# Performance work log

Hardware: AMD Instinct MI355X
Metric: run time of the kernel (lower is better)

Reference implementation:

```python
import jax, jax.numpy as jnp
import numpy as np


def setup_inputs() -> dict:
    key = jax.random.key(0)
    ks = jax.random.split(key, 10)
    B, T, E = 4096, 200, 64
    H0, H1, H2 = 80, 40, 1
    D = 4 * E  # concat feature dim = 256
    glorot = lambda k, shp: jax.random.normal(k, shp, jnp.float32) * jnp.sqrt(2.0 / (shp[0] + shp[1]))
    return {
        "queries": jax.random.normal(ks[0], (B, 1, E), jnp.float32),
        "keys": jax.random.normal(ks[1], (B, T, E), jnp.float32),
        "keys_length": jax.random.randint(ks[2], (B, 1), 0, T, jnp.int32),
        "W0": glorot(ks[3], (D, H0)),
        "b0": jnp.zeros((H0,), jnp.float32),
        "W1": glorot(ks[4], (H0, H1)),
        "b1": jnp.zeros((H1,), jnp.float32),
        "W2": glorot(ks[5], (H1, H2)),
        "b2": jnp.zeros((H2,), jnp.float32),
    }


def reference(queries, keys, keys_length, W0, b0, W1, b1, W2, b2):
    B, T, E = keys.shape
    # repeat query along history axis: [B,1,E] -> [B,T,E]
    q = jnp.broadcast_to(queries, (B, T, E))
    # DIN attention input: [B,T,4E]
    att = jnp.concatenate([q, keys, q - keys, q * keys], axis=-1)
    # tiny 3-layer MLP, sigmoid activations (att_activation, no output_activation override)
    h = jax.nn.sigmoid(att @ W0 + b0)
    h = jax.nn.sigmoid(h @ W1 + b1)
    score = jax.nn.sigmoid(h @ W2 + b2)          # [B,T,1]
    out = jnp.transpose(score, (0, 2, 1))         # [B,1,T]
    # sequence mask: [B,1,T]
    key_masks = jnp.arange(T)[None, None, :] < keys_length[:, :, None]
    # weight_normalization=False -> masked positions become 0, no softmax
    out = jnp.where(key_masks, out, jnp.zeros_like(out))
    # weighted sum over history: [B,1,T] @ [B,T,E] -> [B,1,E]
    return jnp.matmul(out, keys)
```

## Files before the change

### kernel.cpp

```cpp
#include <hip/hip_runtime.h>

#define NT 512
#define NWAVE 8
#define PE 136
#define PW1 104
#define PH 104

typedef __attribute__((ext_vector_type(8))) short short8;
typedef __attribute__((ext_vector_type(4))) float f32x4;

#define DPP_ADD(x, ctrl)                                                    \
  ((x) + __uint_as_float(__builtin_amdgcn_mov_dpp(                          \
             __float_as_uint(x), (ctrl), 0xf, 0xf, true)))

__device__ __forceinline__ unsigned short f2b(float f) {
  unsigned int x = __float_as_uint(f);
  return (unsigned short)((x + 0x7fffu + ((x >> 16) & 1u)) >> 16);
}
__device__ __forceinline__ float b2f(unsigned short u) {
  return __uint_as_float(((unsigned int)u) << 16);
}
__device__ __forceinline__ float sigmoidf(float x) {
  return __builtin_amdgcn_rcpf(1.0f + __expf(-x));
}
__device__ __forceinline__ short8 pack8(float4 a, float4 b) {
  short8 r;
  r[0] = (short)f2b(a.x); r[1] = (short)f2b(a.y); r[2] = (short)f2b(a.z); r[3] = (short)f2b(a.w);
  r[4] = (short)f2b(b.x); r[5] = (short)f2b(b.y); r[6] = (short)f2b(b.z); r[7] = (short)f2b(b.w);
  return r;
}
__device__ __forceinline__ short8 pack8qb(float4 a, float4 b, short8 qp) {
  short8 r;
  r[0] = (short)f2b(a.x * b2f((unsigned short)qp[0]));
  r[1] = (short)f2b(a.y * b2f((unsigned short)qp[1]));
  r[2] = (short)f2b(a.z * b2f((unsigned short)qp[2]));
  r[3] = (short)f2b(a.w * b2f((unsigned short)qp[3]));
  r[4] = (short)f2b(b.x * b2f((unsigned short)qp[4]));
  r[5] = (short)f2b(b.y * b2f((unsigned short)qp[5]));
  r[6] = (short)f2b(b.z * b2f((unsigned short)qp[6]));
  r[7] = (short)f2b(b.w * b2f((unsigned short)qp[7]));
  return r;
}

__global__ __launch_bounds__(256, 2) void prep_c(
    const float* __restrict__ q, const float* __restrict__ W0,
    const float* __restrict__ b0, float* __restrict__ C, int B)
{
  __shared__ float Wac[64 * 80];
  __shared__ float qlds[32 * 64];
  const int bbase = blockIdx.x * 32, tid = threadIdx.x;
  for (int idx = tid; idx < 5120; idx += 256) {
    const int e = idx / 80, h = idx - e * 80;
    Wac[idx] = W0[e * 80 + h] + W0[(128 + e) * 80 + h];
  }
  for (int idx = tid; idx < 2048; idx += 256) {
    const int bl = idx >> 6, e = idx & 63;
    const int bg = bbase + bl;
    qlds[idx] = (bg < B) ? q[bg * 64 + e] : 0.0f;
  }
  __syncthreads();
  #pragma unroll
  for (int i = 0; i < 10; ++i) {
    const int idx = tid + i * 256;
    const int bl = idx / 80, h = idx - bl * 80;
    const int bg = bbase + bl;
    if (bg < B) {
      float acc = b0[h];
      #pragma unroll 8
      for (int e = 0; e < 64; ++e) acc += qlds[bl * 64 + e] * Wac[e * 80 + h];
      C[bg * 80 + h] = acc;
    }
  }
}

#define L1_NT(nt)                                                            \
  {                                                                          \
    const int col = (nt) * 16 + lm;                                          \
    const unsigned short* wr = &WxT[col * PE + quad * 8];                    \
    const short8 w0 = *(const short8*)(wr);                                  \
    const short8 w1 = *(const short8*)(wr + 32);                             \
    const short8 w2 = *(const short8*)(wr + 64);                             \
    const short8 w3 = *(const short8*)(wr + 96);                             \
    f32x4 acc;                                                               \
    acc[0] = cfv[nt]; acc[1] = cfv[nt]; acc[2] = cfv[nt]; acc[3] = cfv[nt];  \
    acc = __builtin_amdgcn_mfma_f32_16x16x32_bf16(a0,  w0, acc, 0, 0, 0);    \
    acc = __builtin_amdgcn_mfma_f32_16x16x32_bf16(a1,  w1, acc, 0, 0, 0);    \
    acc = __builtin_amdgcn_mfma_f32_16x16x32_bf16(aq0, w2, acc, 0, 0, 0);    \
    acc = __builtin_amdgcn_mfma_f32_16x16x32_bf16(aq1, w3, acc, 0, 0, 0);    \
    _Pragma("unroll")                                                        \
    for (int r = 0; r < 4; ++r)                                              \
      h0[(quad * 4 + r) * PH + col] = f2b(sigmoidf(acc[r]));                 \
  }

__global__ __launch_bounds__(NT, 2) void din_attn_main(
    const float* __restrict__ q,
    const float* __restrict__ keys,
    const int* __restrict__ klen,
    const float* __restrict__ W0,
    const float* __restrict__ b0,
    const float* __restrict__ W1,
    const float* __restrict__ b1,
    const float* __restrict__ W2,
    const float* __restrict__ b2,
    float* __restrict__ out,
    const float* __restrict__ Cpre,
    int B)
{
  __shared__ __align__(16) unsigned short WxT[80 * PE];
  __shared__ __align__(16) unsigned short W1T[48 * PW1];
  __shared__ __align__(16) unsigned short h0s[NWAVE][16 * PH];

  const int tid = threadIdx.x;

  for (int idx = tid; idx < 128 * 80; idx += NT) {
    const int e = idx / 80, h = idx - e * 80;
    const float v = (e < 64)
        ? (W0[(64 + e) * 80 + h] - W0[(128 + e) * 80 + h])
        : W0[(128 + e) * 80 + h];
    WxT[h * PE + e] = f2b(v);
  }
  for (int idx = tid; idx < 48 * PW1; idx += NT) {
    const int j = idx / PW1, h = idx - j * PW1;
    W1T[idx] = (j < 40 && h < 80) ? f2b(W1[h * 40 + j]) : (unsigned short)0;
  }
  {
    const int w0i = tid >> 6, ln = tid & 63;
    for (int i = ln; i < 256; i += 64)
      h0s[w0i][(i >> 4) * PH + 80 + (i & 15)] = 0;
  }
  __syncthreads();

  const int wv = __builtin_amdgcn_readfirstlane(tid >> 6);
  const int lane = tid & 63;
  const int lm = lane & 15;
  const int quad = lane >> 4;
  const int b = blockIdx.x * NWAVE + wv;
  if (b >= B) return;

  int L = klen[b];
  L = __builtin_amdgcn_readfirstlane(max(0, min(200, L)));
  unsigned short* h0 = h0s[wv];

  const float4* q4 = (const float4*)(q + (size_t)b * 64);
  const short8 qpk0 = pack8(q4[quad * 2], q4[quad * 2 + 1]);
  const short8 qpk1 = pack8(q4[8 + quad * 2], q4[8 + quad * 2 + 1]);

  float cfv[5];
  if (Cpre != nullptr) {
    #pragma unroll
    for (int nt = 0; nt < 5; ++nt) cfv[nt] = Cpre[b * 80 + nt * 16 + lm];
  } else {
    #pragma unroll
    for (int nt = 0; nt < 5; ++nt) cfv[nt] = b0[nt * 16 + lm];
    for (int e = 0; e < 64; ++e) {
      const float qv = q[(size_t)b * 64 + e];
      #pragma unroll
      for (int nt = 0; nt < 5; ++nt) {
        const int col = nt * 16 + lm;
        cfv[nt] += qv * (W0[e * 80 + col] + W0[(128 + e) * 80 + col]);
      }
    }
  }
  float b1v[3], w2v[3];
  #pragma unroll
  for (int nt = 0; nt < 3; ++nt) {
    const int col = nt * 16 + lm;
    b1v[nt] = (col < 40) ? b1[col] : 0.0f;
    w2v[nt] = (col < 40) ? W2[col] : 0.0f;
  }
  const float b2v = b2[0];
  const short8 z8 = {0, 0, 0, 0, 0, 0, 0, 0};
  const float4 z4 = {0.0f, 0.0f, 0.0f, 0.0f};

  const float* kb = keys + (size_t)b * 12800;
  float4 w4 = {0.0f, 0.0f, 0.0f, 0.0f};
  const int passes = (L + 15) >> 4;

  float4 k0 = z4, k1 = z4, k2 = z4, k3 = z4;
  if (passes > 0 && lm < L) {
    const float4* kp = (const float4*)(kb + (size_t)lm * 64);
    k0 = kp[quad * 2]; k1 = kp[quad * 2 + 1];
    k2 = kp[8 + quad * 2]; k3 = kp[8 + quad * 2 + 1];
  }

  for (int p = 0; p < passes; ++p) {
    const int t0 = p << 4;

    short8 a0 = pack8(k0, k1), a1 = pack8(k2, k3);
    short8 aq0 = pack8qb(k0, k1, qpk0), aq1 = pack8qb(k2, k3, qpk1);
    if (!((t0 + lm) < L)) { a0 = z8; a1 = z8; aq0 = z8; aq1 = z8; }

    float4 kv[4];
    #pragma unroll
    for (int r = 0; r < 4; ++r)
      kv[r] = *(const float4*)(kb + (size_t)min(t0 + 4 * quad + r, 199) * 64 + 4 * lm);

    if (p + 1 < passes) {
      const int t = t0 + 16 + lm;
      if (t < L) {
        const float4* kp = (const float4*)(kb + (size_t)t * 64);
        k0 = kp[quad * 2]; k1 = kp[quad * 2 + 1];
        k2 = kp[8 + quad * 2]; k3 = kp[8 + quad * 2 + 1];
      } else { k0 = z4; k1 = z4; k2 = z4; k3 = z4; }
    }

    __builtin_amdgcn_s_setprio(1);
    L1_NT(0)
    L1_NT(1)
    const short8 ha0 = *(const short8*)&h0[lm * PH + quad * 8];
    L1_NT(2)
    L1_NT(3)
    L1_NT(4)
    __builtin_amdgcn_s_setprio(0);

    const short8 ha1 = *(const short8*)&h0[lm * PH + 32 + quad * 8];
    const short8 ha2 = *(const short8*)&h0[lm * PH + 64 + quad * 8];
    float pd[4] = {0.0f, 0.0f, 0.0f, 0.0f};
    __builtin_amdgcn_s_setprio(1);
    #pragma unroll
    for (int nt = 0; nt < 3; ++nt) {
      const int col = nt * 16 + lm;
      const unsigned short* wr = &W1T[col * PW1 + quad * 8];
      const short8 wb0 = *(const short8*)(wr);
      const short8 wb1 = *(const short8*)(wr + 32);
      const short8 wb2 = *(const short8*)(wr + 64);
      f32x4 acc;
      acc[0] = b1v[nt]; acc[1] = b1v[nt]; acc[2] = b1v[nt]; acc[3] = b1v[nt];
      acc = __builtin_amdgcn_mfma_f32_16x16x32_bf16(ha0, wb0, acc, 0, 0, 0);
      acc = __builtin_amdgcn_mfma_f32_16x16x32_bf16(ha1, wb1, acc, 0, 0, 0);
      acc = __builtin_amdgcn_mfma_f32_16x16x32_bf16(ha2, wb2, acc, 0, 0, 0);
      #pragma unroll
      for (int r = 0; r < 4; ++r) pd[r] += sigmoidf(acc[r]) * w2v[nt];
    }
    __builtin_amdgcn_s_setprio(0);

    #pragma unroll
    for (int r = 0; r < 4; ++r) {
      pd[r] = DPP_ADD(pd[r], 0xB1);
      pd[r] = DPP_ADD(pd[r], 0x4E);
      pd[r] = DPP_ADD(pd[r], 0x141);
      pd[r] = DPP_ADD(pd[r], 0x140);
    }
    float sc[4];
    #pragma unroll
    for (int r = 0; r < 4; ++r) {
      const int ta = t0 + 4 * quad + r;
      sc[r] = (ta < L) ? sigmoidf(pd[r] + b2v) : 0.0f;
    }

    #pragma unroll
    for (int r = 0; r < 4; ++r) {
      w4.x += sc[r] * kv[r].x; w4.y += sc[r] * kv[r].y;
      w4.z += sc[r] * kv[r].z; w4.w += sc[r] * kv[r].w;
    }
  }

  w4.x += __shfl_xor(w4.x, 16); w4.y += __shfl_xor(w4.y, 16);
  w4.z += __shfl_xor(w4.z, 16); w4.w += __shfl_xor(w4.w, 16);
  w4.x += __shfl_xor(w4.x, 32); w4.y += __shfl_xor(w4.y, 32);
  w4.z += __shfl_xor(w4.z, 32); w4.w += __shfl_xor(w4.w, 32);
  if (lane < 16)
    *(float4*)(out + (size_t)b * 64 + 4 * lm) = w4;
}

extern "C" void kernel_launch(void* const* d_in, const int* in_sizes, int n_in,
                              void* d_out, int out_size, void* d_ws, size_t ws_size,
                              hipStream_t stream) {
  const int B = in_sizes[2];
  const float* Cpre = nullptr;
  if (ws_size >= (size_t)B * 80 * sizeof(float)) {
    float* C = (float*)d_ws;
    prep_c<<<(B + 31) / 32, 256, 0, stream>>>(
        (const float*)d_in[0], (const float*)d_in[3], (const float*)d_in[4], C, B);
    Cpre = C;
  }
  din_attn_main<<<(B + NWAVE - 1) / NWAVE, NT, 0, stream>>>(
      (const float*)d_in[0], (const float*)d_in[1], (const int*)d_in[2],
      (const float*)d_in[3], (const float*)d_in[4], (const float*)d_in[5],
      (const float*)d_in[6], (const float*)d_in[7], (const float*)d_in[8],
      (float*)d_out, Cpre, B);
}
```

Baseline: 321.4 us.

## Split each batch row across two waves and sort batches by history length

Assigns two waves per batch row, each handling alternate 16-step passes, and combines their partial weighted sums with atomic adds into a zeroed output. A single-block counting sort orders batch rows by descending key length so that waves in the same block have similar work. The aim is better load balance and more parallelism for variable-length histories. It adds a memset, a serial single-block sort kernel, float atomics with non-deterministic summation order, and duplicated per-row setup work in both waves.

```diff
diff --git a/kernel.cpp b/kernel.cpp
--- a/kernel.cpp
+++ b/kernel.cpp
@@ -70,6 +70,33 @@
       for (int e = 0; e < 64; ++e) acc += qlds[bl * 64 + e] * Wac[e * 80 + h];
       C[bg * 80 + h] = acc;
     }
+  }
+}
+
+__global__ __launch_bounds__(256) void sort_batches(
+    const int* __restrict__ klen, int* __restrict__ order, int B)
+{
+  __shared__ int hist[256];
+  __shared__ int base[256];
+  const int tid = threadIdx.x;
+  hist[tid] = 0;
+  __syncthreads();
+  for (int b = tid; b < B; b += 256) {
+    int L = klen[b];
+    L = max(0, min(200, L));
+    atomicAdd(&hist[L], 1);
+  }
+  __syncthreads();
+  if (tid == 0) {
+    int run = 0;
+    for (int v = 200; v >= 0; --v) { base[v] = run; run += hist[v]; }
+  }
+  __syncthreads();
+  for (int b = tid; b < B; b += 256) {
+    int L = klen[b];
+    L = max(0, min(200, L));
+    const int pos = atomicAdd(&base[L], 1);
+    order[pos] = b;
   }
 }
 
@@ -104,6 +131,7 @@
     const float* __restrict__ b2,
     float* __restrict__ out,
     const float* __restrict__ Cpre,
+    const int* __restrict__ order,
     int B)
 {
   __shared__ __align__(16) unsigned short WxT[80 * PE];
@@ -134,12 +162,15 @@
   const int lane = tid & 63;
   const int lm = lane & 15;
   const int quad = lane >> 4;
-  const int b = blockIdx.x * NWAVE + wv;
-  if (b >= B) return;
+  const int gw = blockIdx.x * NWAVE + wv;
+  const int bidx = gw >> 1;
+  const int half = gw & 1;
+  if (bidx >= B) return;
+  const int b = (order != nullptr) ? order[bidx] : bidx;
+  unsigned short* h0 = h0s[wv];
 
   int L = klen[b];
   L = __builtin_amdgcn_readfirstlane(max(0, min(200, L)));
-  unsigned short* h0 = h0s[wv];
 
   const float4* q4 = (const float4*)(q + (size_t)b * 64);
   const short8 qpk0 = pack8(q4[quad * 2], q4[quad * 2 + 1]);
@@ -177,13 +208,16 @@
   const int passes = (L + 15) >> 4;
 
   float4 k0 = z4, k1 = z4, k2 = z4, k3 = z4;
-  if (passes > 0 && lm < L) {
-    const float4* kp = (const float4*)(kb + (size_t)lm * 64);
-    k0 = kp[quad * 2]; k1 = kp[quad * 2 + 1];
-    k2 = kp[8 + quad * 2]; k3 = kp[8 + quad * 2 + 1];
-  }
-
-  for (int p = 0; p < passes; ++p) {
+  if (half < passes) {
+    const int t = (half << 4) + lm;
+    if (t < L) {
+      const float4* kp = (const float4*)(kb + (size_t)t * 64);
+      k0 = kp[quad * 2]; k1 = kp[quad * 2 + 1];
+      k2 = kp[8 + quad * 2]; k3 = kp[8 + quad * 2 + 1];
+    }
+  }
+
+  for (int p = half; p < passes; p += 2) {
     const int t0 = p << 4;
 
     short8 a0 = pack8(k0, k1), a1 = pack8(k2, k3);
@@ -195,8 +229,8 @@
     for (int r = 0; r < 4; ++r)
       kv[r] = *(const float4*)(kb + (size_t)min(t0 + 4 * quad + r, 199) * 64 + 4 * lm);
 
-    if (p + 1 < passes) {
-      const int t = t0 + 16 + lm;
+    if (p + 2 < passes) {
+      const int t = t0 + 32 + lm;
       if (t < L) {
         const float4* kp = (const float4*)(kb + (size_t)t * 64);
         k0 = kp[quad * 2]; k1 = kp[quad * 2 + 1];
@@ -259,24 +293,39 @@
   w4.z += __shfl_xor(w4.z, 16); w4.w += __shfl_xor(w4.w, 16);
   w4.x += __shfl_xor(w4.x, 32); w4.y += __shfl_xor(w4.y, 32);
   w4.z += __shfl_xor(w4.z, 32); w4.w += __shfl_xor(w4.w, 32);
-  if (lane < 16)
-    *(float4*)(out + (size_t)b * 64 + 4 * lm) = w4;
+  if (lane < 16) {
+    float* op = out + (size_t)b * 64 + 4 * lm;
+    atomicAdd(op + 0, w4.x); atomicAdd(op + 1, w4.y);
+    atomicAdd(op + 2, w4.z); atomicAdd(op + 3, w4.w);
+  }
 }
 
 extern "C" void kernel_launch(void* const* d_in, const int* in_sizes, int n_in,
                               void* d_out, int out_size, void* d_ws, size_t ws_size,
                               hipStream_t stream) {
   const int B = in_sizes[2];
+  const size_t csize = (size_t)B * 80 * sizeof(float);
+  const size_t csize_al = (csize + 255) & ~(size_t)255;
+  const size_t osize = (size_t)B * sizeof(int);
+
   const float* Cpre = nullptr;
-  if (ws_size >= (size_t)B * 80 * sizeof(float)) {
-    float* C = (float*)d_ws;
+  int* order = nullptr;
+  if (ws_size >= csize) Cpre = (const float*)d_ws;
+  if (ws_size >= csize_al + osize) order = (int*)((char*)d_ws + csize_al);
+
+  hipMemsetAsync(d_out, 0, (size_t)out_size, stream);
+  if (order != nullptr) {
+    sort_batches<<<1, 256, 0, stream>>>((const int*)d_in[2], order, B);
+  }
+  if (Cpre != nullptr) {
     prep_c<<<(B + 31) / 32, 256, 0, stream>>>(
-        (const float*)d_in[0], (const float*)d_in[3], (const float*)d_in[4], C, B);
-    Cpre = C;
-  }
-  din_attn_main<<<(B + NWAVE - 1) / NWAVE, NT, 0, stream>>>(
+        (const float*)d_in[0], (const float*)d_in[3], (const float*)d_in[4],
+        (float*)d_ws, B);
+  }
+  const int nwaves = 2 * B;
+  din_attn_main<<<(nwaves + NWAVE - 1) / NWAVE, NT, 0, stream>>>(
       (const float*)d_in[0], (const float*)d_in[1], (const int*)d_in[2],
       (const float*)d_in[3], (const float*)d_in[4], (const float*)d_in[5],
       (const float*)d_in[6], (const float*)d_in[7], (const float*)d_in[8],
-      (float*)d_out, Cpre, B);
-}
+      (float*)d_out, Cpre, order, B);
+}
```

Result: slower. 350.2 us (+9.0%).
